# Performance work log

Hardware: AMD Instinct MI355X
Metric: run time of the kernel (lower is better)

## Reference

```python
import jax, jax.numpy as jnp
import numpy as np

T, IN_SZ, OUT_SZ = 512, 1024, 1024
INIT_TAU = 2.0   # sig_tau = sigmoid(init_tau) is the leak factor
V_TH = 1.0


def setup_inputs() -> dict:
    key = jax.random.key(0)
    k1, k2 = jax.random.split(key)
    x_seq = jax.random.normal(k1, (T, IN_SZ), jnp.float32)
    kernel = jax.random.normal(k2, (IN_SZ, OUT_SZ), jnp.float32) / np.float32(np.sqrt(IN_SZ))
    u0 = jnp.zeros((OUT_SZ,), jnp.float32)
    E0 = jnp.zeros((IN_SZ, OUT_SZ), jnp.float32)  # eligibility trace, same shape as kernel
    return {"x_seq": x_seq, "kernel": kernel, "u0": u0, "E0": E0}


def reference(x_seq, kernel, u0, E0):
    # Forward pass of the OSTL-wrapped spiking cell over a sequence.
    # Primal path (f): LIF dynamics with soft reset; E is not touched in primal.
    sig_tau = jax.nn.sigmoid(jnp.float32(INIT_TAU))
    vth = jnp.float32(V_TH)

    def body(u, x):
        u_new = sig_tau * u + x @ kernel          # [OUT_SZ]
        s = (u_new > vth).astype(x.dtype)          # heaviside spike
        u_out = u_new - s * vth                    # soft reset
        return u_out, s

    u_final, spikes = jax.lax.scan(body, u0, x_seq)  # spikes: [T, OUT_SZ]
    return spikes, u_final
```

## Files before the change

### kernel.cpp

```cpp
#include <hip/hip_runtime.h>
#include <stdint.h>


#define T_STEPS 512
#define IN_SZ   1024
#define OUT_SZ  1024

#define BM 128
#define BN 128
#define BK 32
#define KSPLIT 8
#define KCHUNK (IN_SZ / KSPLIT)
#define NITER  (KCHUNK / BK)

typedef __attribute__((address_space(1))) const void gvoid;
typedef __attribute__((address_space(3))) void lvoid;

__global__ __launch_bounds__(256) void ostl_gemm_splitk(const float* __restrict__ X,
                                                        const float* __restrict__ W,
                                                        float* __restrict__ P) {
    __shared__ float As[2][BK][BM];
    __shared__ float Bs[2][BK * BN];

    const int tid = threadIdx.x;
    const int tx = tid & 15;
    const int ty = tid >> 4;
    const int n0 = blockIdx.x * BN;
    const int m0 = blockIdx.y * BM;
    const int kc = blockIdx.z;
    const int kb = kc * KCHUNK;

    const int am = tid >> 1;
    const int ak = (tid & 1) * 16;
    const int wv = tid >> 6;
    const int ln = tid & 63;

    const float* Arow = X + (size_t)(m0 + am) * IN_SZ + kb + ak;

    float4 areg[4];

    #pragma unroll
    for (int q = 0; q < 4; ++q)
        areg[q] = *reinterpret_cast<const float4*>(Arow + q * 4);
    #pragma unroll
    for (int j = 0; j < 4; ++j) {
        const int i = wv * 4 + j;
        const float* src = W + (size_t)(kb + 2 * i + (ln >> 5)) * OUT_SZ + n0 + (ln & 31) * 4;
        __builtin_amdgcn_global_load_lds((gvoid*)src, (lvoid*)&Bs[0][i * 256], 16, 0, 0);
    }
    {
        float t[16];
        #pragma unroll
        for (int q = 0; q < 4; ++q) *reinterpret_cast<float4*>(&t[q * 4]) = areg[q];
        #pragma unroll
        for (int c = 0; c < 16; ++c) As[0][ak + c][am] = t[c];
    }
    __syncthreads();

    float acc[8][8];
    #pragma unroll
    for (int r = 0; r < 8; ++r)
        #pragma unroll
        for (int c = 0; c < 8; ++c) acc[r][c] = 0.f;

    #pragma unroll 1
    for (int it = 0; it < NITER; ++it) {
        const int cur = it & 1;
        const int nxt = cur ^ 1;

        if (it < NITER - 1) {
            const int kbase = kb + (it + 1) * BK;
            #pragma unroll
            for (int j = 0; j < 4; ++j) {
                const int i = wv * 4 + j;
                const float* src = W + (size_t)(kbase + 2 * i + (ln >> 5)) * OUT_SZ + n0 + (ln & 31) * 4;
                __builtin_amdgcn_global_load_lds((gvoid*)src, (lvoid*)&Bs[nxt][i * 256], 16, 0, 0);
            }
            #pragma unroll
            for (int q = 0; q < 4; ++q)
                areg[q] = *reinterpret_cast<const float4*>(Arow + (it + 1) * BK + q * 4);
        }

        #pragma unroll 8
        for (int k = 0; k < BK; ++k) {
            const float4 a0 = *reinterpret_cast<const float4*>(&As[cur][k][ty * 8]);
            const float4 a1 = *reinterpret_cast<const float4*>(&As[cur][k][ty * 8 + 4]);
            const float4 b0 = *reinterpret_cast<const float4*>(&Bs[cur][k * BN + tx * 4]);
            const float4 b1 = *reinterpret_cast<const float4*>(&Bs[cur][k * BN + tx * 4 + 64]);
            const float av[8] = {a0.x, a0.y, a0.z, a0.w, a1.x, a1.y, a1.z, a1.w};
            const float bv[8] = {b0.x, b0.y, b0.z, b0.w, b1.x, b1.y, b1.z, b1.w};
            #pragma unroll
            for (int r = 0; r < 8; ++r)
                #pragma unroll
                for (int c = 0; c < 8; ++c)
                    acc[r][c] = fmaf(av[r], bv[c], acc[r][c]);
        }

        if (it < NITER - 1) {
            float t[16];
            #pragma unroll
            for (int q = 0; q < 4; ++q) *reinterpret_cast<float4*>(&t[q * 4]) = areg[q];
            #pragma unroll
            for (int c = 0; c < 16; ++c) As[nxt][ak + c][am] = t[c];
            __syncthreads();
        }
    }

    float* Pb = P + (size_t)kc * T_STEPS * OUT_SZ + (size_t)(m0 + ty * 8) * OUT_SZ + n0;
    #pragma unroll
    for (int r = 0; r < 8; ++r) {
        *reinterpret_cast<float4*>(&Pb[(size_t)r * OUT_SZ + tx * 4]) =
            make_float4(acc[r][0], acc[r][1], acc[r][2], acc[r][3]);
        *reinterpret_cast<float4*>(&Pb[(size_t)r * OUT_SZ + tx * 4 + 64]) =
            make_float4(acc[r][4], acc[r][5], acc[r][6], acc[r][7]);
    }
}

__device__ inline float4 f4add(float4 a, float4 b) {
    return make_float4(a.x + b.x, a.y + b.y, a.z + b.z, a.w + b.w);
}

__global__ __launch_bounds__(256) void ostl_reduce8(const float* __restrict__ P,
                                                    float* __restrict__ Y) {
    const size_t idx = ((size_t)blockIdx.x * 256 + threadIdx.x) * 4;
    float4 s[8];
    #pragma unroll
    for (int c = 0; c < 8; ++c)
        s[c] = *reinterpret_cast<const float4*>(P + (size_t)c * T_STEPS * OUT_SZ + idx);
    const float4 t0 = f4add(s[0], s[1]);
    const float4 t1 = f4add(s[2], s[3]);
    const float4 t2 = f4add(s[4], s[5]);
    const float4 t3 = f4add(s[6], s[7]);
    *reinterpret_cast<float4*>(Y + idx) = f4add(f4add(t0, t1), f4add(t2, t3));
}

#define TB 16

__global__ __launch_bounds__(64) void ostl_scan_kernel(const float* __restrict__ u0,
                                                       const float* __restrict__ Yin,
                                                       float* __restrict__ Sout,
                                                       float* __restrict__ u_final) {
    const int j = blockIdx.x * blockDim.x + threadIdx.x;
    if (j >= OUT_SZ) return;

    const float  sig_f   = (float)0.8807970779778823;
    const double sig_tau = (double)sig_f;

    double u = (double)u0[j];
    const float* pin = Yin + j;
    float* pout = Sout + j;

    float bA[TB], bB[TB];

    #pragma unroll
    for (int i = 0; i < TB; ++i) bA[i] = pin[(size_t)i * OUT_SZ];

    #pragma unroll 1
    for (int blk = 0; blk < T_STEPS / TB; blk += 2) {
        #pragma unroll
        for (int i = 0; i < TB; ++i)
            bB[i] = pin[(size_t)((blk + 1) * TB + i) * OUT_SZ];

        #pragma unroll
        for (int i = 0; i < TB; ++i) {
            u = fma(sig_tau, u, (double)bA[i]);
            const float s = (u > 1.0) ? 1.0f : 0.0f;
            pout[(size_t)(blk * TB + i) * OUT_SZ] = s;
            u -= (double)s;
        }

        if (blk + 2 < T_STEPS / TB) {
            #pragma unroll
            for (int i = 0; i < TB; ++i)
                bA[i] = pin[(size_t)((blk + 2) * TB + i) * OUT_SZ];
        }

        #pragma unroll
        for (int i = 0; i < TB; ++i) {
            u = fma(sig_tau, u, (double)bB[i]);
            const float s = (u > 1.0) ? 1.0f : 0.0f;
            pout[(size_t)((blk + 1) * TB + i) * OUT_SZ] = s;
            u -= (double)s;
        }
    }
    u_final[j] = (float)u;
}

extern "C" void kernel_launch(void* const* d_in, const int* in_sizes, int n_in,
                              void* d_out, int out_size, void* d_ws, size_t ws_size,
                              hipStream_t stream) {
    const float* x_seq  = (const float*)d_in[0];
    const float* kernel = (const float*)d_in[1];
    const float* u0     = (const float*)d_in[2];

    float* out      = (float*)d_out;
    float* spikes   = out;
    float* u_final  = out + (size_t)T_STEPS * OUT_SZ;

    float* partials = (float*)d_ws;
    float* yb       = partials + (size_t)KSPLIT * T_STEPS * OUT_SZ;

    dim3 ggrid(OUT_SZ / BN, T_STEPS / BM, KSPLIT);
    ostl_gemm_splitk<<<ggrid, dim3(256), 0, stream>>>(x_seq, kernel, partials);

    ostl_reduce8<<<dim3((T_STEPS * OUT_SZ / 4) / 256), dim3(256), 0, stream>>>(partials, yb);

    ostl_scan_kernel<<<dim3(OUT_SZ / 64), dim3(64), 0, stream>>>(u0, yb, spikes, u_final);
}
```

Baseline: 112.4 us.

## Fuse split-K partial reduction into the sequential LIF scan kernel

Removes the separate reduce kernel and has the scan kernel read all eight split-K partials directly, summing them in registers before each time step. This drops one launch and the write and re-read of the reduced intermediate buffer. In exchange the scan, which runs on only 16 blocks of 64 threads, now issues eight times as many loads, so it may become more latency-bound. The spike reset is rewritten as a select, the prefetch block is halved, and the GEMM inner loop unroll is also reduced.

```diff
diff --git a/kernel.cpp b/kernel.cpp
--- a/kernel.cpp
+++ b/kernel.cpp
@@ -81,7 +81,7 @@
                 areg[q] = *reinterpret_cast<const float4*>(Arow + (it + 1) * BK + q * 4);
         }
 
-        #pragma unroll 8
+        #pragma unroll 4
         for (int k = 0; k < BK; ++k) {
             const float4 a0 = *reinterpret_cast<const float4*>(&As[cur][k][ty * 8]);
             const float4 a1 = *reinterpret_cast<const float4*>(&As[cur][k][ty * 8 + 4]);
@@ -116,71 +116,86 @@
     }
 }
 
-__device__ inline float4 f4add(float4 a, float4 b) {
-    return make_float4(a.x + b.x, a.y + b.y, a.z + b.z, a.w + b.w);
-}
-
-__global__ __launch_bounds__(256) void ostl_reduce8(const float* __restrict__ P,
-                                                    float* __restrict__ Y) {
-    const size_t idx = ((size_t)blockIdx.x * 256 + threadIdx.x) * 4;
-    float4 s[8];
-    #pragma unroll
-    for (int c = 0; c < 8; ++c)
-        s[c] = *reinterpret_cast<const float4*>(P + (size_t)c * T_STEPS * OUT_SZ + idx);
-    const float4 t0 = f4add(s[0], s[1]);
-    const float4 t1 = f4add(s[2], s[3]);
-    const float4 t2 = f4add(s[4], s[5]);
-    const float4 t3 = f4add(s[6], s[7]);
-    *reinterpret_cast<float4*>(Y + idx) = f4add(f4add(t0, t1), f4add(t2, t3));
-}
-
-#define TB 16
-
-__global__ __launch_bounds__(64) void ostl_scan_kernel(const float* __restrict__ u0,
-                                                       const float* __restrict__ Yin,
-                                                       float* __restrict__ Sout,
-                                                       float* __restrict__ u_final) {
-    const int j = blockIdx.x * blockDim.x + threadIdx.x;
-    if (j >= OUT_SZ) return;
+#define TB 8
+
+__global__ __launch_bounds__(64) void ostl_scan_fused(const float* __restrict__ u0,
+                                                      const float* __restrict__ P,
+                                                      float* __restrict__ Sout,
+                                                      float* __restrict__ u_final) {
+    const int j = blockIdx.x * 64 + threadIdx.x;
+    const size_t CS = (size_t)T_STEPS * OUT_SZ;
 
     const float  sig_f   = (float)0.8807970779778823;
     const double sig_tau = (double)sig_f;
 
     double u = (double)u0[j];
-    const float* pin = Yin + j;
+    const float* p = P + j;
     float* pout = Sout + j;
 
-    float bA[TB], bB[TB];
-
-    #pragma unroll
-    for (int i = 0; i < TB; ++i) bA[i] = pin[(size_t)i * OUT_SZ];
+    float rawA[TB][8], rawB[TB][8];
+
+    #pragma unroll
+    for (int i = 0; i < TB; ++i)
+        #pragma unroll
+        for (int c = 0; c < 8; ++c)
+            rawA[i][c] = p[c * CS + (size_t)i * OUT_SZ];
+
+    float yA[TB], yB[TB];
+    #pragma unroll
+    for (int i = 0; i < TB; ++i) {
+        const float t0 = rawA[i][0] + rawA[i][1], t1 = rawA[i][2] + rawA[i][3];
+        const float t2 = rawA[i][4] + rawA[i][5], t3 = rawA[i][6] + rawA[i][7];
+        yA[i] = (t0 + t1) + (t2 + t3);
+    }
 
     #pragma unroll 1
     for (int blk = 0; blk < T_STEPS / TB; blk += 2) {
         #pragma unroll
         for (int i = 0; i < TB; ++i)
-            bB[i] = pin[(size_t)((blk + 1) * TB + i) * OUT_SZ];
+            #pragma unroll
+            for (int c = 0; c < 8; ++c)
+                rawB[i][c] = p[c * CS + (size_t)((blk + 1) * TB + i) * OUT_SZ];
 
         #pragma unroll
         for (int i = 0; i < TB; ++i) {
-            u = fma(sig_tau, u, (double)bA[i]);
-            const float s = (u > 1.0) ? 1.0f : 0.0f;
-            pout[(size_t)(blk * TB + i) * OUT_SZ] = s;
-            u -= (double)s;
+            const double un = fma(sig_tau, u, (double)yA[i]);
+            const double us = un - 1.0;
+            const bool   sp = un > 1.0;
+            pout[(size_t)(blk * TB + i) * OUT_SZ] = sp ? 1.0f : 0.0f;
+            u = sp ? us : un;
+        }
+
+        #pragma unroll
+        for (int i = 0; i < TB; ++i) {
+            const float t0 = rawB[i][0] + rawB[i][1], t1 = rawB[i][2] + rawB[i][3];
+            const float t2 = rawB[i][4] + rawB[i][5], t3 = rawB[i][6] + rawB[i][7];
+            yB[i] = (t0 + t1) + (t2 + t3);
         }
 
         if (blk + 2 < T_STEPS / TB) {
             #pragma unroll
             for (int i = 0; i < TB; ++i)
-                bA[i] = pin[(size_t)((blk + 2) * TB + i) * OUT_SZ];
+                #pragma unroll
+                for (int c = 0; c < 8; ++c)
+                    rawA[i][c] = p[c * CS + (size_t)((blk + 2) * TB + i) * OUT_SZ];
         }
 
         #pragma unroll
         for (int i = 0; i < TB; ++i) {
-            u = fma(sig_tau, u, (double)bB[i]);
-            const float s = (u > 1.0) ? 1.0f : 0.0f;
-            pout[(size_t)((blk + 1) * TB + i) * OUT_SZ] = s;
-            u -= (double)s;
+            const double un = fma(sig_tau, u, (double)yB[i]);
+            const double us = un - 1.0;
+            const bool   sp = un > 1.0;
+            pout[(size_t)((blk + 1) * TB + i) * OUT_SZ] = sp ? 1.0f : 0.0f;
+            u = sp ? us : un;
+        }
+
+        if (blk + 2 < T_STEPS / TB) {
+            #pragma unroll
+            for (int i = 0; i < TB; ++i) {
+                const float t0 = rawA[i][0] + rawA[i][1], t1 = rawA[i][2] + rawA[i][3];
+                const float t2 = rawA[i][4] + rawA[i][5], t3 = rawA[i][6] + rawA[i][7];
+                yA[i] = (t0 + t1) + (t2 + t3);
+            }
         }
     }
     u_final[j] = (float)u;
@@ -198,12 +213,9 @@
     float* u_final  = out + (size_t)T_STEPS * OUT_SZ;
 
     float* partials = (float*)d_ws;
-    float* yb       = partials + (size_t)KSPLIT * T_STEPS * OUT_SZ;
 
     dim3 ggrid(OUT_SZ / BN, T_STEPS / BM, KSPLIT);
     ostl_gemm_splitk<<<ggrid, dim3(256), 0, stream>>>(x_seq, kernel, partials);
 
-    ostl_reduce8<<<dim3((T_STEPS * OUT_SZ / 4) / 256), dim3(256), 0, stream>>>(partials, yb);
-
-    ostl_scan_kernel<<<dim3(OUT_SZ / 64), dim3(64), 0, stream>>>(u0, yb, spikes, u_final);
+    ostl_scan_fused<<<dim3(OUT_SZ / 64), dim3(64), 0, stream>>>(u0, partials, spikes, u_final);
 }
```

Result: slower. 137.5 us (+22.3%).

## Scan each output neuron with a full wavefront using lane shuffles

Applied to the files above, without the earlier changes.

The scan kernel changes from 16 blocks of 64 threads, one neuron per thread, to 1024 wavefronts, one per neuron. Each wave loads all 512 timesteps for its neuron up front (8 per lane), then every lane runs the same serial recurrence redundantly, broadcasting each input with a shuffle. This exposes more parallelism across CUs and hides load latency better than the old 16-block launch. The cost is strided, uncoalesced loads and stores (each lane touches a different row) and a shuffle added to every serial step of the dependent chain.

```diff
diff --git a/kernel.cpp b/kernel.cpp
--- a/kernel.cpp
+++ b/kernel.cpp
@@ -134,56 +134,42 @@
     *reinterpret_cast<float4*>(Y + idx) = f4add(f4add(t0, t1), f4add(t2, t3));
 }
 
-#define TB 16
-
-__global__ __launch_bounds__(64) void ostl_scan_kernel(const float* __restrict__ u0,
-                                                       const float* __restrict__ Yin,
-                                                       float* __restrict__ Sout,
-                                                       float* __restrict__ u_final) {
-    const int j = blockIdx.x * blockDim.x + threadIdx.x;
-    if (j >= OUT_SZ) return;
+__global__ __launch_bounds__(64) void ostl_scan_wave(const float* __restrict__ u0,
+                                                     const float* __restrict__ Y,
+                                                     float* __restrict__ Sout,
+                                                     float* __restrict__ u_final) {
+    const int j = blockIdx.x;
+    const int l = threadIdx.x;
 
     const float  sig_f   = (float)0.8807970779778823;
     const double sig_tau = (double)sig_f;
 
+    float y[8];
+    #pragma unroll
+    for (int q = 0; q < 8; ++q)
+        y[q] = Y[(size_t)(q * 64 + l) * OUT_SZ + j];
+
     double u = (double)u0[j];
-    const float* pin = Yin + j;
-    float* pout = Sout + j;
-
-    float bA[TB], bB[TB];
+    float spk[8];
 
     #pragma unroll
-    for (int i = 0; i < TB; ++i) bA[i] = pin[(size_t)i * OUT_SZ];
-
-    #pragma unroll 1
-    for (int blk = 0; blk < T_STEPS / TB; blk += 2) {
+    for (int q = 0; q < 8; ++q) {
         #pragma unroll
-        for (int i = 0; i < TB; ++i)
-            bB[i] = pin[(size_t)((blk + 1) * TB + i) * OUT_SZ];
-
-        #pragma unroll
-        for (int i = 0; i < TB; ++i) {
-            u = fma(sig_tau, u, (double)bA[i]);
-            const float s = (u > 1.0) ? 1.0f : 0.0f;
-            pout[(size_t)(blk * TB + i) * OUT_SZ] = s;
-            u -= (double)s;
-        }
-
-        if (blk + 2 < T_STEPS / TB) {
-            #pragma unroll
-            for (int i = 0; i < TB; ++i)
-                bA[i] = pin[(size_t)((blk + 2) * TB + i) * OUT_SZ];
-        }
-
-        #pragma unroll
-        for (int i = 0; i < TB; ++i) {
-            u = fma(sig_tau, u, (double)bB[i]);
-            const float s = (u > 1.0) ? 1.0f : 0.0f;
-            pout[(size_t)((blk + 1) * TB + i) * OUT_SZ] = s;
-            u -= (double)s;
+        for (int i = 0; i < 64; ++i) {
+            const float  yv = __shfl(y[q], i, 64);
+            const double un = fma(sig_tau, u, (double)yv);
+            const double us = un - 1.0;
+            const bool   sp = un > 1.0;
+            const float  s  = sp ? 1.0f : 0.0f;
+            if (i == l) spk[q] = s;
+            u = sp ? us : un;
         }
     }
-    u_final[j] = (float)u;
+
+    #pragma unroll
+    for (int q = 0; q < 8; ++q)
+        Sout[(size_t)(q * 64 + l) * OUT_SZ + j] = spk[q];
+    if (l == 0) u_final[j] = (float)u;
 }
 
 extern "C" void kernel_launch(void* const* d_in, const int* in_sizes, int n_in,
@@ -205,5 +191,5 @@
 
     ostl_reduce8<<<dim3((T_STEPS * OUT_SZ / 4) / 256), dim3(256), 0, stream>>>(partials, yb);
 
-    ostl_scan_kernel<<<dim3(OUT_SZ / 64), dim3(64), 0, stream>>>(u0, yb, spikes, u_final);
+    ostl_scan_wave<<<dim3(OUT_SZ), dim3(64), 0, stream>>>(u0, yb, spikes, u_final);
 }
```

Measured after the change: 115.5 us. 2.7% more time.
